# Optimization experiments

Hardware: AMD Instinct MI355X
Metric: run time of the kernel (lower is better)

The kernel has to match this reference:

```python
import jax, jax.numpy as jnp
import numpy as np

L, D, T, B = 4, 256, 4096, 8  # n_layer, hidden, seq_len, batch


def setup_inputs() -> dict:
    key = jax.random.key(0)
    ks = jax.random.split(key, 12)
    x = jax.random.normal(ks[0], (B, T, D), dtype=jnp.float32)
    # stable LRU diagonal init: |lambda| in [0.9, 0.999], phase in [0, pi/10]
    r = jax.random.uniform(ks[1], (L, D), minval=0.9, maxval=0.999)
    nu_log = jnp.log(-jnp.log(r))
    theta = jax.random.uniform(ks[2], (L, D), minval=1e-4, maxval=np.pi / 10)
    theta_log = jnp.log(theta)
    gamma_log = 0.5 * jnp.log(1.0 - r ** 2)  # normalization gamma = sqrt(1-|lam|^2)
    s = 0.02  # matches truncated_normal_init std
    B_re = s * jax.random.normal(ks[3], (L, D, D), dtype=jnp.float32)
    B_im = s * jax.random.normal(ks[4], (L, D, D), dtype=jnp.float32)
    C_re = s * jax.random.normal(ks[5], (L, D, D), dtype=jnp.float32)
    C_im = s * jax.random.normal(ks[6], (L, D, D), dtype=jnp.float32)
    D_vec = s * jax.random.normal(ks[7], (L, D), dtype=jnp.float32)
    Wg = s * jax.random.normal(ks[8], (L, D, D), dtype=jnp.float32)
    ln_scale = jnp.ones((L, D), dtype=jnp.float32)
    ln_bias = jnp.zeros((L, D), dtype=jnp.float32)
    return dict(x=x, nu_log=nu_log, theta_log=theta_log, gamma_log=gamma_log,
                B_re=B_re, B_im=B_im, C_re=C_re, C_im=C_im, D_vec=D_vec,
                Wg=Wg, ln_scale=ln_scale, ln_bias=ln_bias)


def _layer_norm(x, scale, bias):
    mu = x.mean(-1, keepdims=True)
    var = x.var(-1, keepdims=True)
    return (x - mu) / jnp.sqrt(var + 1e-5) * scale + bias


def _lru_scan(lam, bu):
    # lam: (D,) complex diagonal transition; bu: (T,B,D) complex inputs
    a = jnp.broadcast_to(lam, bu.shape)

    def comb(e1, e2):
        a1, b1 = e1
        a2, b2 = e2
        return a1 * a2, a2 * b1 + b2

    _, h = jax.lax.associative_scan(comb, (a, bu), axis=0)
    return h  # (T,B,D) complex


def reference(x, nu_log, theta_log, gamma_log, B_re, B_im, C_re, C_im, D_vec, Wg, ln_scale, ln_bias):
    u = jnp.transpose(x, (1, 0, 2))  # time-major (T,B,D), mirrors torch permute(1,0,2)
    for l in range(L):  # fixed small layer loop
        z = _layer_norm(u, ln_scale[l], ln_bias[l])
        lam = jnp.exp(-jnp.exp(nu_log[l]) + 1j * jnp.exp(theta_log[l]))  # (D,)
        Bm = B_re[l] + 1j * B_im[l]
        bu = jnp.einsum('tbd,ed->tbe', z.astype(jnp.complex64), Bm) * jnp.exp(gamma_log[l])
        h = _lru_scan(lam, bu)  # (T,B,D) complex state (h0 = 0, matching get_zero_internal_state)
        y = jnp.einsum('tbe,de->tbd', h, C_re[l] + 1j * C_im[l]).real + D_vec[l] * z
        y = y * jax.nn.sigmoid(jnp.einsum('tbd,ed->tbe', z, Wg[l]))  # gating=True output gate
        u = u + y  # residual
    return jnp.transpose(u, (1, 0, 2))  # back to (B,T,D)
```

## Files before the change

### kernel.cpp

```cpp
#include <hip/hip_runtime.h>
#include <hip/hip_bf16.h>

#define NLAYER 4
#define DDIM 256
#define TSEQ 4096
#define NBATCH 8
#define MROWS (NBATCH * TSEQ)
#define CLEN 32
#define NCHUNK (TSEQ / CLEN)

typedef float f32x4 __attribute__((ext_vector_type(4)));
typedef short bf16x8 __attribute__((ext_vector_type(8)));

__device__ __forceinline__ float bf2f(unsigned short u) {
    union { unsigned int i; float f; } v; v.i = ((unsigned int)u) << 16; return v.f;
}
__device__ __forceinline__ unsigned short f2bf(float f) {
    union { float f; unsigned int i; } v; v.f = f;
    unsigned int r = v.i + 0x7fffu + ((v.i >> 16) & 1u);
    return (unsigned short)(r >> 16);
}

__device__ __forceinline__ void gload16(const unsigned short* g, unsigned short* l) {
    __builtin_amdgcn_global_load_lds(
        (const __attribute__((address_space(1))) unsigned int*)g,
        (__attribute__((address_space(3))) unsigned int*)l, 16, 0, 0);
}

__global__ __launch_bounds__(256) void prepack_kernel(
    const float* __restrict__ nu_log, const float* __restrict__ theta_log,
    const float* __restrict__ gamma_log,
    const float* __restrict__ B_re, const float* __restrict__ B_im,
    const float* __restrict__ C_re, const float* __restrict__ C_im,
    const float* __restrict__ Wg,
    unsigned short* __restrict__ wBre, unsigned short* __restrict__ wBim,
    unsigned short* __restrict__ wWg, unsigned short* __restrict__ wCre,
    unsigned short* __restrict__ wCimn,
    float* __restrict__ lam_re, float* __restrict__ lam_im,
    float* __restrict__ lamC_re, float* __restrict__ lamC_im)
{
    int idx = blockIdx.x * 256 + threadIdx.x;
    const int total = NLAYER * DDIM * DDIM;
    if (idx < total) {
        int l = idx >> 16;
        int e = (idx >> 8) & 255;
        float gam = expf(gamma_log[l * DDIM + e]);
        wBre[idx]  = f2bf(B_re[idx] * gam);
        wBim[idx]  = f2bf(B_im[idx] * gam);
        wWg[idx]   = f2bf(Wg[idx]);
        wCre[idx]  = f2bf(C_re[idx]);
        wCimn[idx] = f2bf(-C_im[idx]);
    }
    if (idx < NLAYER * DDIM) {
        float mag = expf(-expf(nu_log[idx]));
        float th  = expf(theta_log[idx]);
        float ar = mag * cosf(th);
        float ai = mag * sinf(th);
        lam_re[idx] = ar;
        lam_im[idx] = ai;
        #pragma unroll
        for (int s = 0; s < 5; ++s) {
            float nr = ar * ar - ai * ai;
            float ni = 2.0f * ar * ai;
            ar = nr; ai = ni;
        }
        lamC_re[idx] = ar;
        lamC_im[idx] = ai;
    }
}

__global__ __launch_bounds__(256) void ln_kernel(
    const float* __restrict__ u, unsigned short* __restrict__ z,
    const float* __restrict__ scale, const float* __restrict__ bias,
    float2* __restrict__ rowStats)
{
    int wid = threadIdx.x >> 6;
    int lane = threadIdx.x & 63;
    int row = blockIdx.x * 4 + wid;
    const float4 v = *reinterpret_cast<const float4*>(u + (size_t)row * DDIM + lane * 4);
    float s  = v.x + v.y + v.z + v.w;
    float s2 = v.x * v.x + v.y * v.y + v.z * v.z + v.w * v.w;
    #pragma unroll
    for (int off = 32; off > 0; off >>= 1) {
        s  += __shfl_xor(s, off);
        s2 += __shfl_xor(s2, off);
    }
    float mu  = s * (1.0f / DDIM);
    float var = s2 * (1.0f / DDIM) - mu * mu;
    float inv = rsqrtf(var + 1e-5f);
    if (lane == 0) { float2 st; st.x = mu; st.y = inv; rowStats[row] = st; }
    float zv[4] = { v.x, v.y, v.z, v.w };
    ushort4 o;
    unsigned short* op = (unsigned short*)&o;
    #pragma unroll
    for (int j = 0; j < 4; ++j) {
        int d = lane * 4 + j;
        op[j] = f2bf((zv[j] - mu) * inv * scale[d] + bias[d]);
    }
    *reinterpret_cast<ushort4*>(z + (size_t)row * DDIM + lane * 4) = o;
}

__global__ __launch_bounds__(256) void gemm1_kernel(
    const unsigned short* __restrict__ z,
    const unsigned short* __restrict__ wBre, const unsigned short* __restrict__ wBim,
    const unsigned short* __restrict__ wWg,
    unsigned short* __restrict__ bure, unsigned short* __restrict__ buim,
    unsigned short* __restrict__ sg,
    const float* __restrict__ lam_re, const float* __restrict__ lam_im,
    float2* __restrict__ fin)
{
    const int n0 = blockIdx.x * 64;
    const int m0 = blockIdx.y * 128;

    __shared__ unsigned short Al[128 * 64];
    __shared__ unsigned short Wl[3][64 * 64];

    const int tid = threadIdx.x;
    const int lane = tid & 63;
    const int wid = tid >> 6;
    const int wr = wid >> 1, wc = wid & 1;
    const int lr = lane >> 3;
    const int lc = lane & 7;

    f32x4 acc[3][4][2] = {};

    for (int ko = 0; ko < 256; ko += 64) {
        #pragma unroll
        for (int it = 0; it < 4; ++it) {
            int s = wid * 4 + it;
            int r = s * 8 + lr;
            int gc = lc ^ (r & 7);
            gload16(z + (size_t)(m0 + r) * 256 + ko + gc * 8, &Al[s * 512]);
        }
        #pragma unroll
        for (int it = 0; it < 2; ++it) {
            int s = wid * 2 + it;
            int r = s * 8 + lr;
            int gc = lc ^ (r & 7);
            size_t off = (size_t)(n0 + r) * 256 + ko + gc * 8;
            gload16(wBre + off, &Wl[0][s * 512]);
            gload16(wBim + off, &Wl[1][s * 512]);
            gload16(wWg  + off, &Wl[2][s * 512]);
        }
        __syncthreads();

        #pragma unroll
        for (int k2 = 0; k2 < 64; k2 += 32) {
            int ac = (k2 >> 3) + (lane >> 4);
            bf16x8 a[4];
            #pragma unroll
            for (int mi = 0; mi < 4; ++mi) {
                int ar = wr * 64 + mi * 16 + (lane & 15);
                a[mi] = *reinterpret_cast<const bf16x8*>(&Al[ar * 64 + ((ac ^ (ar & 7)) * 8)]);
            }
            int br0 = wc * 32 + (lane & 15);
            int br1 = br0 + 16;
            #pragma unroll
            for (int mat = 0; mat < 3; ++mat) {
                bf16x8 b0 = *reinterpret_cast<const bf16x8*>(&Wl[mat][br0 * 64 + ((ac ^ (br0 & 7)) * 8)]);
                bf16x8 b1 = *reinterpret_cast<const bf16x8*>(&Wl[mat][br1 * 64 + ((ac ^ (br1 & 7)) * 8)]);
                #pragma unroll
                for (int mi = 0; mi < 4; ++mi) {
                    acc[mat][mi][0] = __builtin_amdgcn_mfma_f32_16x16x32_bf16(a[mi], b0, acc[mat][mi][0], 0, 0, 0);
                    acc[mat][mi][1] = __builtin_amdgcn_mfma_f32_16x16x32_bf16(a[mi], b1, acc[mat][mi][1], 0, 0, 0);
                }
            }
        }
        __syncthreads();
    }

    unsigned short* Tre = Al;
    unsigned short* Tim = &Wl[0][0];
    #pragma unroll
    for (int mat = 0; mat < 3; ++mat) {
        unsigned short* out = (mat == 0) ? bure : ((mat == 1) ? buim : sg);
        #pragma unroll
        for (int mi = 0; mi < 4; ++mi) {
            #pragma unroll
            for (int ni = 0; ni < 2; ++ni) {
                int cl = wc * 32 + ni * 16 + (lane & 15);
                int rl = wr * 64 + mi * 16 + (lane >> 4) * 4;
                #pragma unroll
                for (int j = 0; j < 4; ++j) {
                    float v = acc[mat][mi][ni][j];
                    unsigned short bv;
                    if (mat == 2) { bv = f2bf(1.0f / (1.0f + expf(-v))); }
                    else          { bv = f2bf(v); }
                    out[(size_t)(m0 + rl + j) * 256 + n0 + cl] = bv;
                    if (mat == 0) Tre[(rl + j) * 64 + cl] = bv;
                    if (mat == 1) Tim[(rl + j) * 64 + cl] = bv;
                }
            }
        }
    }
    __syncthreads();
    {
        const int c = tid >> 6;
        const int col = tid & 63;
        const int dglob = n0 + col;
        const float lr_ = lam_re[dglob], li_ = lam_im[dglob];
        float hr = 0.0f, hi = 0.0f;
        #pragma unroll 8
        for (int k = 0; k < CLEN; ++k) {
            int row = c * 32 + k;
            float br = bf2f(Tre[row * 64 + col]);
            float bi = bf2f(Tim[row * 64 + col]);
            float nr = fmaf(lr_, hr, fmaf(-li_, hi, br));
            float ni = fmaf(lr_, hi, fmaf(li_, hr, bi));
            hr = nr; hi = ni;
        }
        const int b = m0 >> 12;
        const int cglob = ((m0 & 4095) >> 5) + c;
        float2 o; o.x = hr; o.y = hi;
        fin[((size_t)b * 256 + dglob) * 128 + cglob] = o;
    }
}

__global__ __launch_bounds__(256) void scan_prefix_kernel(
    const float2* __restrict__ fin, float2* __restrict__ pre,
    const float* __restrict__ lamC_re, const float* __restrict__ lamC_im)
{
    const int lane = threadIdx.x & 63;
    const int w = blockIdx.x * 4 + (threadIdx.x >> 6);
    const int d = w & 255;
    const float ar = lamC_re[d], ai = lamC_im[d];
    const float4 f = *reinterpret_cast<const float4*>(fin + (size_t)w * 128 + lane * 2);
    const float f0r = f.x, f0i = f.y, f1r = f.z, f1i = f.w;
    float Tr = fmaf(ar, f0r, fmaf(-ai, f0i, f1r));
    float Ti = fmaf(ar, f0i, fmaf(ai, f0r, f1i));
    float Ar_ = ar * ar - ai * ai;
    float Ai_ = 2.0f * ar * ai;
    #pragma unroll
    for (int s = 1; s < 64; s <<= 1) {
        float ur = __shfl_up(Tr, s, 64);
        float ui = __shfl_up(Ti, s, 64);
        if (lane >= s) {
            Tr = fmaf(Ar_, ur, fmaf(-Ai_, ui, Tr));
            Ti = fmaf(Ar_, ui, fmaf(Ai_, ur, Ti));
        }
        float nr = Ar_ * Ar_ - Ai_ * Ai_;
        float ni = 2.0f * Ar_ * Ai_;
        Ar_ = nr; Ai_ = ni;
    }
    float Er = __shfl_up(Tr, 1, 64);
    float Ei = __shfl_up(Ti, 1, 64);
    if (lane == 0) { Er = 0.0f; Ei = 0.0f; }
    float P1r = fmaf(ar, Er, fmaf(-ai, Ei, f0r));
    float P1i = fmaf(ar, Ei, fmaf(ai, Er, f0i));
    float4 o; o.x = Er; o.y = Ei; o.z = P1r; o.w = P1i;
    *reinterpret_cast<float4*>(pre + (size_t)w * 128 + lane * 2) = o;
}

__global__ __launch_bounds__(256) void gemm2_kernel(
    const unsigned short* __restrict__ bure, const unsigned short* __restrict__ buim,
    const unsigned short* __restrict__ wCre, const unsigned short* __restrict__ wCimn,
    const unsigned short* __restrict__ sg, const float2* __restrict__ pre,
    const float* __restrict__ lam_re, const float* __restrict__ lam_im,
    const float* __restrict__ scale, const float* __restrict__ bias,
    const float2* __restrict__ rowStats,
    const float* __restrict__ Dv, const float* __restrict__ uin, float* __restrict__ uout)
{
    const int m0 = blockIdx.x * 64;

    __shared__ unsigned short Ar[64 * 64];
    __shared__ unsigned short Ai[64 * 64];
    __shared__ unsigned short Cr[256 * 64];
    __shared__ unsigned short Ci[256 * 64];

    const int tid = threadIdx.x;
    const int lane = tid & 63;
    const int wid = tid >> 6;
    const int lr = lane >> 3;
    const int lc = lane & 7;

    const int b = m0 >> 12;
    const int cbase = (m0 & 4095) >> 5;

    f32x4 acc[4][4] = {};

    for (int ko = 0; ko < 256; ko += 64) {
        #pragma unroll
        for (int it = 0; it < 2; ++it) {
            int s = wid * 2 + it;
            int r = s * 8 + lr;
            int gc = lc ^ (r & 7);
            size_t off = (size_t)(m0 + r) * 256 + ko + gc * 8;
            gload16(bure + off, &Ar[s * 512]);
            gload16(buim + off, &Ai[s * 512]);
        }
        #pragma unroll
        for (int it = 0; it < 8; ++it) {
            int s = wid * 8 + it;
            int r = s * 8 + lr;
            int gc = lc ^ (r & 7);
            size_t off = (size_t)r * 256 + ko + gc * 8;
            gload16(wCre + off, &Cr[s * 512]);
            gload16(wCimn + off, &Ci[s * 512]);
        }
        __syncthreads();

        if (tid < 128) {
            const int c = tid >> 6;
            const int dl = tid & 63;
            const int dg = ko + dl;
            const float lre = lam_re[dg], lim = lam_im[dg];
            float2 p = pre[((size_t)b * 256 + dg) * 128 + cbase + c];
            float hr = p.x, hi = p.y;
            #pragma unroll 8
            for (int k = 0; k < CLEN; ++k) {
                int row = c * 32 + k;
                int off = row * 64 + (((dl >> 3) ^ (row & 7)) * 8) + (dl & 7);
                float br = bf2f(Ar[off]);
                float bi = bf2f(Ai[off]);
                float nr = fmaf(lre, hr, fmaf(-lim, hi, br));
                float ni = fmaf(lre, hi, fmaf(lim, hr, bi));
                hr = nr; hi = ni;
                Ar[off] = f2bf(nr);
                Ai[off] = f2bf(ni);
            }
        }
        __syncthreads();

        #pragma unroll
        for (int k2 = 0; k2 < 64; k2 += 32) {
            int ac = (k2 >> 3) + (lane >> 4);
            bf16x8 are[4], aim[4];
            #pragma unroll
            for (int mi = 0; mi < 4; ++mi) {
                int arow = mi * 16 + (lane & 15);
                int idx = arow * 64 + ((ac ^ (arow & 7)) * 8);
                are[mi] = *reinterpret_cast<const bf16x8*>(&Ar[idx]);
                aim[mi] = *reinterpret_cast<const bf16x8*>(&Ai[idx]);
            }
            #pragma unroll
            for (int ni = 0; ni < 4; ++ni) {
                int brow = wid * 64 + ni * 16 + (lane & 15);
                int ib = brow * 64 + ((ac ^ (brow & 7)) * 8);
                bf16x8 bre = *reinterpret_cast<const bf16x8*>(&Cr[ib]);
                bf16x8 bim = *reinterpret_cast<const bf16x8*>(&Ci[ib]);
                #pragma unroll
                for (int mi = 0; mi < 4; ++mi) {
                    acc[mi][ni] = __builtin_amdgcn_mfma_f32_16x16x32_bf16(are[mi], bre, acc[mi][ni], 0, 0, 0);
                    acc[mi][ni] = __builtin_amdgcn_mfma_f32_16x16x32_bf16(aim[mi], bim, acc[mi][ni], 0, 0, 0);
                }
            }
        }
        __syncthreads();
    }

    #pragma unroll
    for (int mi = 0; mi < 4; ++mi) {
        #pragma unroll
        for (int ni = 0; ni < 4; ++ni) {
            int col = wid * 64 + ni * 16 + (lane & 15);
            int mrow = m0 + mi * 16 + (lane >> 4) * 4;
            float dv = Dv[col];
            float scc = scale[col], bcc = bias[col];
            #pragma unroll
            for (int j = 0; j < 4; ++j) {
                size_t idx = (size_t)(mrow + j) * 256 + col;
                float2 st = rowStats[mrow + j];
                float uv = uin[idx];
                float zz = (uv - st.x) * st.y * scc + bcc;
                float s = bf2f(sg[idx]);
                uout[idx] = uv + (acc[mi][ni][j] + dv * zz) * s;
            }
        }
    }
}

extern "C" void kernel_launch(void* const* d_in, const int* in_sizes, int n_in,
                              void* d_out, int out_size, void* d_ws, size_t ws_size,
                              hipStream_t stream) {
    const float* x         = (const float*)d_in[0];
    const float* nu_log    = (const float*)d_in[1];
    const float* theta_log = (const float*)d_in[2];
    const float* gamma_log = (const float*)d_in[3];
    const float* B_re      = (const float*)d_in[4];
    const float* B_im      = (const float*)d_in[5];
    const float* C_re      = (const float*)d_in[6];
    const float* C_im      = (const float*)d_in[7];
    const float* D_vec     = (const float*)d_in[8];
    const float* Wg        = (const float*)d_in[9];
    const float* ln_scale  = (const float*)d_in[10];
    const float* ln_bias   = (const float*)d_in[11];
    float* out = (float*)d_out;

    const size_t MSZ = (size_t)MROWS * DDIM;
    const size_t WSZ = (size_t)NLAYER * DDIM * DDIM;
    const size_t FSZ = (size_t)NBATCH * DDIM * NCHUNK;

    unsigned short* b16 = (unsigned short*)d_ws;
    unsigned short* z     = b16;
    unsigned short* sg    = b16 + MSZ;
    unsigned short* bure  = b16 + 2 * MSZ;
    unsigned short* buim  = b16 + 3 * MSZ;
    unsigned short* wBre  = b16 + 4 * MSZ;
    unsigned short* wBim  = wBre + WSZ;
    unsigned short* wWg   = wBim + WSZ;
    unsigned short* wCre  = wWg + WSZ;
    unsigned short* wCimn = wCre + WSZ;
    float* lam_re  = (float*)(wCimn + WSZ);
    float* lam_im  = lam_re + NLAYER * DDIM;
    float* lamC_re = lam_im + NLAYER * DDIM;
    float* lamC_im = lamC_re + NLAYER * DDIM;
    float2* fin = (float2*)(lamC_im + NLAYER * DDIM);
    float2* pre = fin + FSZ;
    float2* rowStats = pre + FSZ;

    prepack_kernel<<<1024, 256, 0, stream>>>(nu_log, theta_log, gamma_log,
                                             B_re, B_im, C_re, C_im, Wg,
                                             wBre, wBim, wWg, wCre, wCimn,
                                             lam_re, lam_im, lamC_re, lamC_im);

    for (int l = 0; l < NLAYER; ++l) {
        const float* uin = (l == 0) ? x : out;
        const float* lre = lam_re + l * DDIM;
        const float* lim = lam_im + l * DDIM;
        ln_kernel<<<MROWS / 4, 256, 0, stream>>>(uin, z, ln_scale + l * DDIM, ln_bias + l * DDIM, rowStats);
        gemm1_kernel<<<dim3(4, MROWS / 128), 256, 0, stream>>>(
            z, wBre + l * DDIM * DDIM, wBim + l * DDIM * DDIM, wWg + l * DDIM * DDIM,
            bure, buim, sg, lre, lim, fin);
        scan_prefix_kernel<<<512, 256, 0, stream>>>(fin, pre,
                                                    lamC_re + l * DDIM, lamC_im + l * DDIM);
        gemm2_kernel<<<MROWS / 64, 256, 0, stream>>>(
            bure, buim, wCre + l * DDIM * DDIM, wCimn + l * DDIM * DDIM,
            sg, pre, lre, lim,
            ln_scale + l * DDIM, ln_bias + l * DDIM, rowStats,
            D_vec + l * DDIM, uin, out);
    }
}
```

Before: 307.3 us.

## Fuse next-layer LayerNorm into gemm2 epilogue and swap gemm1 grid order

gemm2 now computes per-row sum and sum-of-squares of the new residual output, reduces them across lanes and waves through shared memory, and writes the next layer's normalized bf16 activations and row stats directly. This removes three standalone LayerNorm launches and their re-read of the fp32 residual; LN now runs only once, up front, for the input. Row stats are double-buffered between layers. gemm1's grid is also transposed so consecutive blocks walk along M instead of N. The fused epilogue adds register pressure (uvals array), extra syncs, and a one-pass variance formula that is slightly less precise.

```diff
diff --git a/kernel.cpp b/kernel.cpp
--- a/kernel.cpp
+++ b/kernel.cpp
@@ -109,8 +109,8 @@
     const float* __restrict__ lam_re, const float* __restrict__ lam_im,
     float2* __restrict__ fin)
 {
-    const int n0 = blockIdx.x * 64;
-    const int m0 = blockIdx.y * 128;
+    const int m0 = blockIdx.x * 128;
+    const int n0 = blockIdx.y * 64;
 
     __shared__ unsigned short Al[128 * 64];
     __shared__ unsigned short Wl[3][64 * 64];
@@ -258,7 +258,9 @@
     const float* __restrict__ lam_re, const float* __restrict__ lam_im,
     const float* __restrict__ scale, const float* __restrict__ bias,
     const float2* __restrict__ rowStats,
-    const float* __restrict__ Dv, const float* __restrict__ uin, float* __restrict__ uout)
+    const float* __restrict__ Dv, const float* __restrict__ uin, float* __restrict__ uout,
+    const float* __restrict__ nscale, const float* __restrict__ nbias,
+    unsigned short* __restrict__ zout, float2* __restrict__ statsOut, int writeLN)
 {
     const int m0 = blockIdx.x * 64;
 
@@ -348,6 +350,13 @@
         __syncthreads();
     }
 
+    float uvals[4][4][4];
+    float rs[4][4], rs2[4][4];
+    #pragma unroll
+    for (int mi = 0; mi < 4; ++mi)
+        #pragma unroll
+        for (int j = 0; j < 4; ++j) { rs[mi][j] = 0.0f; rs2[mi][j] = 0.0f; }
+
     #pragma unroll
     for (int mi = 0; mi < 4; ++mi) {
         #pragma unroll
@@ -363,7 +372,65 @@
                 float uv = uin[idx];
                 float zz = (uv - st.x) * st.y * scc + bcc;
                 float s = bf2f(sg[idx]);
-                uout[idx] = uv + (acc[mi][ni][j] + dv * zz) * s;
+                float o = uv + (acc[mi][ni][j] + dv * zz) * s;
+                uout[idx] = o;
+                uvals[mi][ni][j] = o;
+                rs[mi][j] += o;
+                rs2[mi][j] += o * o;
+            }
+        }
+    }
+
+    if (writeLN) {
+        #pragma unroll
+        for (int mi = 0; mi < 4; ++mi)
+            #pragma unroll
+            for (int j = 0; j < 4; ++j)
+                #pragma unroll
+                for (int off = 1; off < 16; off <<= 1) {
+                    rs[mi][j]  += __shfl_xor(rs[mi][j], off);
+                    rs2[mi][j] += __shfl_xor(rs2[mi][j], off);
+                }
+        float* sS   = (float*)Ar;
+        float* sS2  = sS + 256;
+        float* sMu  = sS2 + 256;
+        float* sInv = sMu + 64;
+        __syncthreads();
+        if ((lane & 15) == 0) {
+            int hi = lane >> 4;
+            #pragma unroll
+            for (int mi = 0; mi < 4; ++mi)
+                #pragma unroll
+                for (int j = 0; j < 4; ++j) {
+                    int row = mi * 16 + hi * 4 + j;
+                    sS[wid * 64 + row]  = rs[mi][j];
+                    sS2[wid * 64 + row] = rs2[mi][j];
+                }
+        }
+        __syncthreads();
+        if (tid < 64) {
+            float s  = sS[tid] + sS[64 + tid] + sS[128 + tid] + sS[192 + tid];
+            float s2 = sS2[tid] + sS2[64 + tid] + sS2[128 + tid] + sS2[192 + tid];
+            float mu  = s * (1.0f / 256.0f);
+            float var = s2 * (1.0f / 256.0f) - mu * mu;
+            float inv = rsqrtf(var + 1e-5f);
+            sMu[tid] = mu; sInv[tid] = inv;
+            float2 st; st.x = mu; st.y = inv;
+            statsOut[m0 + tid] = st;
+        }
+        __syncthreads();
+        #pragma unroll
+        for (int mi = 0; mi < 4; ++mi) {
+            #pragma unroll
+            for (int ni = 0; ni < 4; ++ni) {
+                int col = wid * 64 + ni * 16 + (lane & 15);
+                float nsc = nscale[col], nbi = nbias[col];
+                #pragma unroll
+                for (int j = 0; j < 4; ++j) {
+                    int row = mi * 16 + (lane >> 4) * 4 + j;
+                    float zz = (uvals[mi][ni][j] - sMu[row]) * sInv[row] * nsc + nbi;
+                    zout[(size_t)(m0 + row) * 256 + col] = f2bf(zz);
+                }
             }
         }
     }
@@ -406,19 +473,24 @@
     float* lamC_im = lamC_re + NLAYER * DDIM;
     float2* fin = (float2*)(lamC_im + NLAYER * DDIM);
     float2* pre = fin + FSZ;
-    float2* rowStats = pre + FSZ;
+    float2* statsA = pre + FSZ;
+    float2* statsB = statsA + MROWS;
 
     prepack_kernel<<<1024, 256, 0, stream>>>(nu_log, theta_log, gamma_log,
                                              B_re, B_im, C_re, C_im, Wg,
                                              wBre, wBim, wWg, wCre, wCimn,
                                              lam_re, lam_im, lamC_re, lamC_im);
 
+    ln_kernel<<<MROWS / 4, 256, 0, stream>>>(x, z, ln_scale, ln_bias, statsA);
+
     for (int l = 0; l < NLAYER; ++l) {
         const float* uin = (l == 0) ? x : out;
         const float* lre = lam_re + l * DDIM;
         const float* lim = lam_im + l * DDIM;
-        ln_kernel<<<MROWS / 4, 256, 0, stream>>>(uin, z, ln_scale + l * DDIM, ln_bias + l * DDIM, rowStats);
-        gemm1_kernel<<<dim3(4, MROWS / 128), 256, 0, stream>>>(
+        float2* statsIn  = (l & 1) ? statsB : statsA;
+        float2* statsOut = (l & 1) ? statsA : statsB;
+        int nl = (l < NLAYER - 1) ? (l + 1) : l;
+        gemm1_kernel<<<dim3(MROWS / 128, 4), 256, 0, stream>>>(
             z, wBre + l * DDIM * DDIM, wBim + l * DDIM * DDIM, wWg + l * DDIM * DDIM,
             bure, buim, sg, lre, lim, fin);
         scan_prefix_kernel<<<512, 256, 0, stream>>>(fin, pre,
@@ -426,7 +498,9 @@
         gemm2_kernel<<<MROWS / 64, 256, 0, stream>>>(
             bure, buim, wCre + l * DDIM * DDIM, wCimn + l * DDIM * DDIM,
             sg, pre, lre, lim,
-            ln_scale + l * DDIM, ln_bias + l * DDIM, rowStats,
-            D_vec + l * DDIM, uin, out);
-    }
-}
+            ln_scale + l * DDIM, ln_bias + l * DDIM, statsIn,
+            D_vec + l * DDIM, uin, out,
+            ln_scale + nl * DDIM, ln_bias + nl * DDIM,
+            z, statsOut, (l < NLAYER - 1) ? 1 : 0);
+    }
+}
```

After: 287.5 us. -6.4%, faster.
